# Kernel optimization log

Hardware: AMD Instinct MI355X
Metric: run time of the kernel (lower is better)

Reference implementation:

```python
import jax, jax.numpy as jnp
import numpy as np

N = 65536      # nodes in batched graph
E = 2097152    # edges (avg degree 32)
V = 1000       # chord vocabulary size
F_IN = 128     # chord feature dim
H = 256        # hidden_dim
OUT = 128      # out_dim
G = 256        # number of graphs in batch


def _gcn_layer(x, W, b, row, col, norm, n):
    # x: [n, f_in] -> [n, f_out]; PyG GCNConv: linear then normalized aggregation + bias
    x = x @ W
    msg = x[row] * norm[:, None]            # gather at source, scale by sym-norm
    return jax.ops.segment_sum(msg, col, num_segments=n) + b


def setup_inputs() -> dict:
    key = jax.random.key(0)
    ks = jax.random.split(key, 9)
    chord_feats = jax.random.normal(ks[0], (V, F_IN), jnp.float32)
    W1 = jax.random.normal(ks[1], (F_IN, H), jnp.float32) * 0.05
    b1 = jnp.zeros((H,), jnp.float32)
    W2 = jax.random.normal(ks[2], (H, OUT), jnp.float32) * 0.05
    b2 = jnp.zeros((OUT,), jnp.float32)
    edge_attr = jax.random.uniform(ks[3], (E,), jnp.float32)          # positive edge weights
    node_indices = jax.random.randint(ks[4], (N,), 0, V, jnp.int64)
    edge_index = jax.random.randint(ks[5], (2, E), 0, N, jnp.int64)
    batch_index = jnp.sort(jax.random.randint(ks[6], (N,), 0, G, jnp.int64))
    return {"chord_feats": chord_feats, "W1": W1, "b1": b1, "W2": W2, "b2": b2,
            "edge_attr": edge_attr, "node_indices": node_indices,
            "edge_index": edge_index, "batch_index": batch_index}


def reference(chord_feats, W1, b1, W2, b2, edge_attr, node_indices, edge_index, batch_index):
    loops = jnp.arange(N, dtype=edge_index.dtype)
    row = jnp.concatenate([edge_index[0], loops])   # source
    col = jnp.concatenate([edge_index[1], loops])   # target
    ew = jnp.concatenate([edge_attr, jnp.ones((N,), edge_attr.dtype)])  # self-loop weight 1
    # symmetric GCN normalization: D^-1/2 A D^-1/2
    deg = jax.ops.segment_sum(ew, col, num_segments=N)
    dis = jnp.where(deg > 0, jax.lax.rsqrt(jnp.maximum(deg, 1e-30)), 0.0)
    norm = dis[row] * ew * dis[col]

    x = chord_feats[node_indices]                   # [N, F_IN]
    x = jax.nn.relu(_gcn_layer(x, W1, b1, row, col, norm, N))
    x = jax.nn.relu(_gcn_layer(x, W2, b2, row, col, norm, N))

    # global_mean_pool over batch_index
    sums = jax.ops.segment_sum(x, batch_index, num_segments=G)
    counts = jax.ops.segment_sum(jnp.ones((N,), x.dtype), batch_index, num_segments=G)
    return sums / jnp.maximum(counts, 1.0)[:, None]
```

## Files before the change

### kernel.cpp

```cpp
#include <hip/hip_runtime.h>
#include <hip/hip_fp16.h>
#include <math.h>

constexpr int N_NODES = 65536;
constexpr int N_EDGES = 2097152;
constexpr int F_IN    = 128;
constexpr int H_DIM   = 256;
constexpr int O_DIM   = 128;
constexpr int N_GRAPH = 256;
constexpr int V_SIZE  = 1000;

constexpr int EPB  = 8192;
constexpr int NBLK = N_EDGES / EPB;
constexpr float FXP = 16777216.0f;

typedef _Float16 half8 __attribute__((ext_vector_type(8)));
typedef float floatx4 __attribute__((ext_vector_type(4)));


__global__ void k_init(float* __restrict__ pool, const int* __restrict__ batch,
                       float* __restrict__ cntf, const float* __restrict__ cf,
                       const float* __restrict__ W1, __half* __restrict__ cfW1,
                       const float* __restrict__ W2, _Float16* __restrict__ W2T) {
    __shared__ float xs[8 * F_IN];
    int i = blockIdx.x * blockDim.x + threadIdx.x;
    if (i < N_GRAPH * O_DIM) pool[i] = 0.0f;
    if (blockIdx.x == 0) {
        int g = threadIdx.x;
        int lo = 0, hi = N_NODES;
        while (lo < hi) { int m = (lo + hi) >> 1; if (batch[m] < g) lo = m + 1; else hi = m; }
        int start = lo;
        lo = 0; hi = N_NODES;
        while (lo < hi) { int m = (lo + hi) >> 1; if (batch[m] <= g) lo = m + 1; else hi = m; }
        cntf[g] = (float)(lo - start);
    }
    if (blockIdx.x < V_SIZE / 8) {
        int rb = blockIdx.x * 8;
        int t  = threadIdx.x;
        #pragma unroll
        for (int p = 0; p < 4; ++p) {
            int idx = p * 256 + t;
            int r = idx >> 7, k = idx & 127;
            xs[idx] = cf[(size_t)(rb + r) * F_IN + k];
        }
        __syncthreads();
        float acc[8] = {};
        for (int k = 0; k < F_IN; ++k) {
            float w = W1[k * H_DIM + t];
            #pragma unroll
            for (int j = 0; j < 8; ++j) acc[j] += xs[j * F_IN + k] * w;
        }
        #pragma unroll
        for (int j = 0; j < 8; ++j)
            cfW1[(size_t)(rb + j) * H_DIM + t] = __float2half(acc[j]);
    }
    if (blockIdx.x >= 128) {
        int idx = (blockIdx.x - 128) * 256 + threadIdx.x;
        int nn = idx >> 8, kk = idx & 255;
        W2T[idx] = (_Float16)W2[kk * O_DIM + nn];
    }
}


__global__ void k_hist(const int* __restrict__ col, int* __restrict__ hist) {
    __shared__ int h[256];
    int t = threadIdx.x;
    if (t < 256) h[t] = 0;
    __syncthreads();
    int base = blockIdx.x * EPB;
    #pragma unroll
    for (int i = 0; i < EPB / 1024; ++i)
        atomicAdd(&h[col[base + i * 1024 + t] >> 8], 1);
    __syncthreads();
    if (t < 256) hist[t * NBLK + blockIdx.x] = h[t];
}


__global__ void k_scan1(const int* __restrict__ in, int* __restrict__ out,
                        int* __restrict__ bsum) {
    __shared__ int s[256];
    int tid = threadIdx.x;
    int i = blockIdx.x * 256 + tid;
    int v = in[i];
    s[tid] = v;
    __syncthreads();
    for (int d = 1; d < 256; d <<= 1) {
        int t = (tid >= d) ? s[tid - d] : 0;
        __syncthreads();
        s[tid] += t;
        __syncthreads();
    }
    out[i] = s[tid] - v;
    if (tid == 255) bsum[blockIdx.x] = s[255];
}

__global__ void k_scan2(int* __restrict__ bsum) {
    __shared__ int s[256];
    int tid = threadIdx.x;
    int v = bsum[tid];
    s[tid] = v;
    __syncthreads();
    for (int d = 1; d < 256; d <<= 1) {
        int t = (tid >= d) ? s[tid - d] : 0;
        __syncthreads();
        s[tid] += t;
        __syncthreads();
    }
    bsum[tid] = s[tid] - v;
}


__global__ void k_part(const int* __restrict__ row, const int* __restrict__ col,
                       const float* __restrict__ ew, const int* __restrict__ nidx,
                       const int* __restrict__ hoffs, const int* __restrict__ bsum,
                       int2* __restrict__ part) {
    __shared__ int cur[256];
    int t = threadIdx.x;
    if (t < 256) cur[t] = hoffs[t * NBLK + blockIdx.x] + bsum[t];
    __syncthreads();
    int base = blockIdx.x * EPB;
    #pragma unroll
    for (int i = 0; i < EPB / 1024; ++i) {
        int e = base + i * 1024 + t;
        int r = row[e], c = col[e];
        unsigned hw = (unsigned)__half_as_ushort(__float2half(ew[e]));
        int vb = nidx[r];
        int slot = atomicAdd(&cur[c >> 8], 1);
        int2 rec;
        rec.x = (r << 16) | ((c & 255) << 8) | (vb >> 2);
        rec.y = (int)(((unsigned)(vb & 3) << 16) | hw);
        part[slot] = rec;
    }
}


__global__ void k_build1(const int* __restrict__ hoffs, const int* __restrict__ bsum,
                         const int2* __restrict__ part, float* __restrict__ dis,
                         int* __restrict__ offs) {
    __shared__ unsigned long long dc[256];
    __shared__ int sc[256];
    int t = threadIdx.x;
    int bucket = blockIdx.x;
    if (t < 256) dc[t] = 0ULL;
    __syncthreads();
    int start = hoffs[bucket * NBLK] + bsum[bucket];
    int end   = (bucket == 255) ? N_EDGES : (hoffs[(bucket + 1) * NBLK] + bsum[bucket + 1]);
    for (int j = start + t; j < end; j += 1024) {
        int2 rec = part[j];
        int dst = (rec.x >> 8) & 255;
        float w = __half2float(__ushort_as_half((unsigned short)(rec.y & 0xFFFF)));
        atomicAdd(&dc[dst], (1ULL << 40) |
                  (unsigned long long)(unsigned)(w * FXP + 0.5f));
    }
    __syncthreads();
    unsigned long long v = (t < 256) ? dc[t] : 0ULL;
    if (t < 256) {
        float deg = 1.0f + (float)(v & 0xFFFFFFFFFFULL) * (1.0f / FXP);
        dis[bucket * 256 + t] = 1.0f / sqrtf(deg);
        sc[t] = (int)(v >> 40);
    }
    __syncthreads();
    for (int d = 1; d < 256; d <<= 1) {
        int x = (t >= d && t < 256) ? sc[t - d] : 0;
        __syncthreads();
        if (t < 256) sc[t] += x;
        __syncthreads();
    }
    if (t < 256) {
        int cnt = (int)(v >> 40);
        offs[bucket * 256 + t] = start + sc[t] - cnt;
    }
    if (bucket == 255 && t == 255) offs[N_NODES] = N_EDGES;
}


__global__ void k_build2(const int* __restrict__ hoffs, const int* __restrict__ bsum,
                         const int2* __restrict__ part, const float* __restrict__ dis,
                         const int* __restrict__ offs, int2* __restrict__ csr) {
    __shared__ int cur[256];
    int t = threadIdx.x;
    int bucket = blockIdx.x;
    if (t < 256) cur[t] = offs[bucket * 256 + t];
    __syncthreads();
    int start = hoffs[bucket * NBLK] + bsum[bucket];
    int end   = (bucket == 255) ? N_EDGES : (hoffs[(bucket + 1) * NBLK] + bsum[bucket + 1]);
    for (int j = start + t; j < end; j += 1024) {
        int2 rec = part[j];
        int dst = (rec.x >> 8) & 255;
        unsigned src = ((unsigned)rec.x) >> 16;
        int vb = ((rec.x & 255) << 2) | ((rec.y >> 16) & 3);
        float w = __half2float(__ushort_as_half((unsigned short)(rec.y & 0xFFFF)));
        float nm = dis[src] * w;
        int slot = atomicAdd(&cur[dst], 1);
        int2 e;
        e.x = (int)((src << 10) | (unsigned)vb);
        e.y = __float_as_int(nm);
        csr[slot] = e;
    }
}

__device__ __forceinline__ void acc8(float* e, int4 v, float n) {
    float2 f0 = __half22float2(*(__half2*)&v.x);
    float2 f1 = __half22float2(*(__half2*)&v.y);
    float2 f2 = __half22float2(*(__half2*)&v.z);
    float2 f3 = __half22float2(*(__half2*)&v.w);
    e[0] += f0.x * n; e[1] += f0.y * n;
    e[2] += f1.x * n; e[3] += f1.y * n;
    e[4] += f2.x * n; e[5] += f2.y * n;
    e[6] += f3.x * n; e[7] += f3.y * n;
}


__global__ void k_agg1(const int4* __restrict__ cfW1, const int* __restrict__ nidx,
                       const float* __restrict__ dis, const int* __restrict__ offs,
                       const int2* __restrict__ csr, const float4* __restrict__ b1f4,
                       int4* __restrict__ h1) {
    int wave = threadIdx.x >> 6;
    int lane = threadIdx.x & 63;
    int g    = lane >> 5;
    int sl   = lane & 31;
    int c = blockIdx.x * 4 + wave;
    float d = dis[c];
    int4 sp = cfW1[(size_t)nidx[c] * 32 + sl];
    float esum[8] = {0.f, 0.f, 0.f, 0.f, 0.f, 0.f, 0.f, 0.f};
    int a0 = offs[c], a1 = offs[c + 1];
    int s = a0;
    if (s < a1 && (s & 1)) {
        int sb = __builtin_amdgcn_readfirstlane(s);
        int2 e0 = csr[sb];
        int4 v0 = cfW1[(size_t)(e0.x & 1023) * 32 + sl];
        float n = (g == 0) ? __int_as_float(e0.y) : 0.0f;
        acc8(esum, v0, n);
        ++s;
    }
    for (; s + 8 <= a1; s += 8) {
        int sb = __builtin_amdgcn_readfirstlane(s);
        int4 ee[4];
        #pragma unroll
        for (int u = 0; u < 4; ++u) ee[u] = *(const int4*)(csr + sb + 2 * u);
        int4 v[4]; float n[4];
        #pragma unroll
        for (int u = 0; u < 4; ++u) {
            int ex = g ? ee[u].z : ee[u].x;
            int ey = g ? ee[u].w : ee[u].y;
            n[u] = __int_as_float(ey);
            v[u] = cfW1[(size_t)(ex & 1023) * 32 + sl];
        }
        #pragma unroll
        for (int u = 0; u < 4; ++u) acc8(esum, v[u], n[u]);
    }
    for (; s + 2 <= a1; s += 2) {
        int sb = __builtin_amdgcn_readfirstlane(s);
        int4 ee = *(const int4*)(csr + sb);
        int ex = g ? ee.z : ee.x;
        int ey = g ? ee.w : ee.y;
        int4 v0 = cfW1[(size_t)(ex & 1023) * 32 + sl];
        acc8(esum, v0, __int_as_float(ey));
    }
    if (s < a1) {
        int sb = __builtin_amdgcn_readfirstlane(s);
        int2 e0 = csr[sb];
        int4 v0 = cfW1[(size_t)(e0.x & 1023) * 32 + sl];
        float n = (g == 0) ? __int_as_float(e0.y) : 0.0f;
        acc8(esum, v0, n);
    }
    #pragma unroll
    for (int k = 0; k < 8; ++k) esum[k] += __shfl_xor(esum[k], 32, 64);

    float dd = d * d;
    float2 s0 = __half22float2(*(__half2*)&sp.x);
    float2 s1 = __half22float2(*(__half2*)&sp.y);
    float2 s2 = __half22float2(*(__half2*)&sp.z);
    float2 s3 = __half22float2(*(__half2*)&sp.w);
    float4 bb0 = b1f4[2 * sl];
    float4 bb1 = b1f4[2 * sl + 1];
    float r[8];
    r[0] = bb0.x + s0.x * dd + d * esum[0];
    r[1] = bb0.y + s0.y * dd + d * esum[1];
    r[2] = bb0.z + s1.x * dd + d * esum[2];
    r[3] = bb0.w + s1.y * dd + d * esum[3];
    r[4] = bb1.x + s2.x * dd + d * esum[4];
    r[5] = bb1.y + s2.y * dd + d * esum[5];
    r[6] = bb1.z + s3.x * dd + d * esum[6];
    r[7] = bb1.w + s3.y * dd + d * esum[7];
    #pragma unroll
    for (int k = 0; k < 8; ++k) r[k] = r[k] > 0.f ? r[k] : 0.f;
    float2 p0 = {r[0], r[1]}, p1 = {r[2], r[3]}, p2 = {r[4], r[5]}, p3 = {r[6], r[7]};
    __half2 h0 = __float22half2_rn(p0);
    __half2 h1v = __float22half2_rn(p1);
    __half2 h2 = __float22half2_rn(p2);
    __half2 h3 = __float22half2_rn(p3);
    int4 outv;
    outv.x = *(int*)&h0;
    outv.y = *(int*)&h1v;
    outv.z = *(int*)&h2;
    outv.w = *(int*)&h3;
    if (lane < 32) h1[(size_t)c * 32 + sl] = outv;
}


__global__ void k_gemm2(const _Float16* __restrict__ h1, const _Float16* __restrict__ W2T,
                        __half* __restrict__ xw2h) {
    int wave = threadIdx.x >> 6;
    int lane = threadIdx.x & 63;
    int quad = lane >> 4;
    int n    = lane & 15;
    int tm   = blockIdx.x * 4 + wave;
    const _Float16* arow = h1 + (size_t)(tm * 16 + n) * H_DIM;
    half8 a[8];
    #pragma unroll
    for (int kt = 0; kt < 8; ++kt)
        a[kt] = *(const half8*)(arow + kt * 32 + quad * 8);
    #pragma unroll
    for (int nt = 0; nt < 8; ++nt) {
        floatx4 acc = {0.f, 0.f, 0.f, 0.f};
        const _Float16* brow = W2T + (size_t)(nt * 16 + n) * H_DIM;
        #pragma unroll
        for (int kt = 0; kt < 8; ++kt) {
            half8 b = *(const half8*)(brow + kt * 32 + quad * 8);
            acc = __builtin_amdgcn_mfma_f32_16x16x32_f16(a[kt], b, acc, 0, 0, 0);
        }
        #pragma unroll
        for (int r = 0; r < 4; ++r) {
            int rowi = tm * 16 + quad * 4 + r;
            xw2h[(size_t)rowi * O_DIM + nt * 16 + n] = __float2half(acc[r]);
        }
    }
}


__global__ void k_agg2_pool(const int4* __restrict__ xw2h, const float* __restrict__ b2,
                            const float* __restrict__ dis, const int* __restrict__ offs,
                            const int2* __restrict__ csr, const int* __restrict__ batch,
                            float* __restrict__ pool) {
    __shared__ float red[4][128];
    __shared__ int bgs[4];
    int wave = threadIdx.x >> 6;
    int lane = threadIdx.x & 63;
    int grp  = lane >> 4;
    int sl   = lane & 15;
    int c = blockIdx.x * 4 + wave;
    float d = dis[c];
    int4 sp = xw2h[(size_t)c * 16 + sl];
    float esum[8] = {0.f, 0.f, 0.f, 0.f, 0.f, 0.f, 0.f, 0.f};
    int s0 = offs[c], s1 = offs[c + 1];
    int s = s0;
    for (; s + 16 <= s1; s += 16) {
        int sb = __builtin_amdgcn_readfirstlane(s);
        int2 e[4];
        #pragma unroll
        for (int u = 0; u < 4; ++u) e[u] = csr[sb + 4 * u + grp];
        int4 v[4];
        #pragma unroll
        for (int u = 0; u < 4; ++u)
            v[u] = xw2h[(size_t)(((unsigned)e[u].x) >> 10) * 16 + sl];
        #pragma unroll
        for (int u = 0; u < 4; ++u) acc8(esum, v[u], __int_as_float(e[u].y));
    }
    for (; s + 4 <= s1; s += 4) {
        int sb = __builtin_amdgcn_readfirstlane(s);
        int2 e0 = csr[sb + grp];
        int4 v0 = xw2h[(size_t)(((unsigned)e0.x) >> 10) * 16 + sl];
        acc8(esum, v0, __int_as_float(e0.y));
    }
    if (s < s1) {
        int sb = __builtin_amdgcn_readfirstlane(s);
        int idx = sb + grp;
        int idc = idx < s1 ? idx : s1 - 1;
        int2 e0 = csr[idc];
        int4 v0 = xw2h[(size_t)(((unsigned)e0.x) >> 10) * 16 + sl];
        float n = (idx < s1) ? __int_as_float(e0.y) : 0.0f;
        acc8(esum, v0, n);
    }
    #pragma unroll
    for (int k = 0; k < 8; ++k) {
        esum[k] += __shfl_xor(esum[k], 16, 64);
        esum[k] += __shfl_xor(esum[k], 32, 64);
    }
    float dd = d * d;
    float2 f0 = __half22float2(*(__half2*)&sp.x);
    float2 f1 = __half22float2(*(__half2*)&sp.y);
    float2 f2 = __half22float2(*(__half2*)&sp.z);
    float2 f3 = __half22float2(*(__half2*)&sp.w);
    float4 bb0 = ((const float4*)b2)[2 * sl];
    float4 bb1 = ((const float4*)b2)[2 * sl + 1];
    float acc[8];
    acc[0] = bb0.x + f0.x * dd + d * esum[0];
    acc[1] = bb0.y + f0.y * dd + d * esum[1];
    acc[2] = bb0.z + f1.x * dd + d * esum[2];
    acc[3] = bb0.w + f1.y * dd + d * esum[3];
    acc[4] = bb1.x + f2.x * dd + d * esum[4];
    acc[5] = bb1.y + f2.y * dd + d * esum[5];
    acc[6] = bb1.z + f3.x * dd + d * esum[6];
    acc[7] = bb1.w + f3.y * dd + d * esum[7];
    #pragma unroll
    for (int k = 0; k < 8; ++k) acc[k] = acc[k] > 0.f ? acc[k] : 0.f;
    if (grp == 0) {
        #pragma unroll
        for (int k = 0; k < 8; ++k) red[wave][8 * sl + k] = acc[k];
    }
    if (lane == 0) bgs[wave] = batch[c];
    __syncthreads();
    if (wave == 0) {
        float2 a;
        a.x = red[0][2 * lane];
        a.y = red[0][2 * lane + 1];
        int cg = bgs[0];
        #pragma unroll
        for (int w = 1; w < 4; ++w) {
            int g = bgs[w];
            float2 r;
            r.x = red[w][2 * lane];
            r.y = red[w][2 * lane + 1];
            if (g == cg) { a.x += r.x; a.y += r.y; }
            else {
                atomicAdd(&pool[cg * O_DIM + 2 * lane], a.x);
                atomicAdd(&pool[cg * O_DIM + 2 * lane + 1], a.y);
                a = r; cg = g;
            }
        }
        atomicAdd(&pool[cg * O_DIM + 2 * lane], a.x);
        atomicAdd(&pool[cg * O_DIM + 2 * lane + 1], a.y);
    }
}

__global__ void k_final(const float* __restrict__ pool, const float* __restrict__ cnt,
                        float* __restrict__ out) {
    int t = blockIdx.x * blockDim.x + threadIdx.x;
    if (t < N_GRAPH * O_DIM) {
        int g = t / O_DIM;
        out[t] = pool[t] / fmaxf(cnt[g], 1.0f);
    }
}


extern "C" void kernel_launch(void* const* d_in, const int* in_sizes, int n_in,
                              void* d_out, int out_size, void* d_ws, size_t ws_size,
                              hipStream_t stream) {
    const float* cf   = (const float*)d_in[0];
    const float* W1   = (const float*)d_in[1];
    const float* b1   = (const float*)d_in[2];
    const float* W2   = (const float*)d_in[3];
    const float* b2   = (const float*)d_in[4];
    const float* ew   = (const float*)d_in[5];
    const int*   nidx = (const int*)d_in[6];
    const int*   eidx = (const int*)d_in[7];
    const int*   bidx = (const int*)d_in[8];
    float* out = (float*)d_out;

    const int* row = eidx;
    const int* col = eidx + N_EDGES;

    char* ws = (char*)d_ws;
    size_t off = 0;
    int*   hist  = (int*)  (ws + off); off += (size_t)N_NODES * 4;
    int*   hoffs = (int*)  (ws + off); off += (size_t)N_NODES * 4;
    int*   bsum  = (int*)  (ws + off); off += 4096;
    float* dis   = (float*)(ws + off); off += (size_t)N_NODES * 4;
    int*   offs  = (int*)  (ws + off); off += (size_t)(N_NODES + 16) * 4;
    int2*  csr   = (int2*) (ws + off); off += (size_t)N_EDGES * 8;
    float* pool  = (float*)(ws + off); off += (size_t)(N_GRAPH * O_DIM + N_GRAPH) * 4;
    __half* cfW1 = (__half*)(ws + off); off += (size_t)V_SIZE * H_DIM * 2;
    _Float16* W2T = (_Float16*)(ws + off); off += (size_t)O_DIM * H_DIM * 2;
    off = (off + 255) & ~(size_t)255;
    int2*  part  = (int2*) (ws + off); off += (size_t)N_EDGES * 8;
    __half* h1   = (__half*)(ws + off);
    __half* xw2h = (__half*)part;
    float* cntf  = pool + N_GRAPH * O_DIM;

    k_init<<<256, 256, 0, stream>>>(pool, bidx, cntf, cf, W1, cfW1, W2, W2T);
    k_hist<<<NBLK, 1024, 0, stream>>>(col, hist);
    k_scan1<<<256, 256, 0, stream>>>(hist, hoffs, bsum);
    k_scan2<<<1, 256, 0, stream>>>(bsum);

    k_part<<<NBLK, 1024, 0, stream>>>(row, col, ew, nidx, hoffs, bsum, part);
    k_build1<<<256, 1024, 0, stream>>>(hoffs, bsum, part, dis, offs);
    k_build2<<<256, 1024, 0, stream>>>(hoffs, bsum, part, dis, offs, csr);

    k_agg1<<<N_NODES / 4, 256, 0, stream>>>((const int4*)cfW1, nidx, dis, offs, csr,
                                            (const float4*)b1, (int4*)h1);

    k_gemm2<<<N_NODES / 64, 256, 0, stream>>>((const _Float16*)h1, W2T, xw2h);
    k_agg2_pool<<<N_NODES / 4, 256, 0, stream>>>((const int4*)xw2h, b2, dis, offs, csr,
                                                 bidx, pool);

    k_final<<<(N_GRAPH * O_DIM + 255) / 256, 256, 0, stream>>>(pool, cntf, out);
}
```

Measured before the change: 321.3 us.

## Split CSR build into quarter-bucket blocks and halve edges per partition block

Halves edges per partition block so twice as many blocks run the histogram and partition passes. The scan is widened to match, with the second scan handling two sums per thread. The degree/offset build kernel is split into three: a degree counter where each bucket is handled by four blocks that each own a quarter of the destinations, a separate per-bucket prefix-scan kernel, and a quarter-bucket CSR scatter. This raises parallelism from 256 to 1024 blocks, but each block now reads the whole bucket's partition and discards three quarters of it. Degree accumulation moves to a 32-bit fixed point with 16 fractional bits, which loses precision and risks overflow if a node's weight sum exceeds 256.

```diff
diff --git a/kernel.cpp b/kernel.cpp
--- a/kernel.cpp
+++ b/kernel.cpp
@@ -10,9 +10,8 @@
 constexpr int N_GRAPH = 256;
 constexpr int V_SIZE  = 1000;
 
-constexpr int EPB  = 8192;
+constexpr int EPB  = 4096;
 constexpr int NBLK = N_EDGES / EPB;
-constexpr float FXP = 16777216.0f;
 
 typedef _Float16 half8 __attribute__((ext_vector_type(8)));
 typedef float floatx4 __attribute__((ext_vector_type(4)));
@@ -96,17 +95,20 @@
 
 __global__ void k_scan2(int* __restrict__ bsum) {
     __shared__ int s[256];
-    int tid = threadIdx.x;
-    int v = bsum[tid];
-    s[tid] = v;
+    int t = threadIdx.x;
+    int2 v = *(int2*)&bsum[2 * t];
+    int tsum = v.x + v.y;
+    s[t] = tsum;
     __syncthreads();
     for (int d = 1; d < 256; d <<= 1) {
-        int t = (tid >= d) ? s[tid - d] : 0;
-        __syncthreads();
-        s[tid] += t;
-        __syncthreads();
-    }
-    bsum[tid] = s[tid] - v;
+        int x = (t >= d) ? s[t - d] : 0;
+        __syncthreads();
+        s[t] += x;
+        __syncthreads();
+    }
+    int ex = s[t] - tsum;
+    bsum[2 * t]     = ex;
+    bsum[2 * t + 1] = ex + v.x;
 }
 
 
@@ -116,7 +118,10 @@
                        int2* __restrict__ part) {
     __shared__ int cur[256];
     int t = threadIdx.x;
-    if (t < 256) cur[t] = hoffs[t * NBLK + blockIdx.x] + bsum[t];
+    if (t < 256) {
+        int idx = t * NBLK + blockIdx.x;
+        cur[t] = hoffs[idx] + bsum[idx >> 8];
+    }
     __syncthreads();
     int base = blockIdx.x * EPB;
     #pragma unroll
@@ -134,68 +139,79 @@
 }
 
 
-__global__ void k_build1(const int* __restrict__ hoffs, const int* __restrict__ bsum,
-                         const int2* __restrict__ part, float* __restrict__ dis,
-                         int* __restrict__ offs) {
-    __shared__ unsigned long long dc[256];
+__global__ void k_degq(const int* __restrict__ hoffs, const int* __restrict__ bsum,
+                       const int2* __restrict__ part, unsigned* __restrict__ dcq) {
+    __shared__ unsigned dc[64];
+    int t = threadIdx.x;
+    int bucket = blockIdx.x & 255, q = blockIdx.x >> 8;
+    if (t < 64) dc[t] = 0u;
+    __syncthreads();
+    int start = hoffs[bucket * NBLK] + bsum[bucket * 2];
+    int end   = (bucket == 255) ? N_EDGES
+                                : (hoffs[(bucket + 1) * NBLK] + bsum[(bucket + 1) * 2]);
+    for (int j = start + t; j < end; j += 1024) {
+        int2 rec = part[j];
+        int dst = (rec.x >> 8) & 255;
+        if ((dst >> 6) == q) {
+            float w = __half2float(__ushort_as_half((unsigned short)(rec.y & 0xFFFF)));
+            atomicAdd(&dc[dst & 63], (1u << 24) | (unsigned)(w * 65536.0f + 0.5f));
+        }
+    }
+    __syncthreads();
+    if (t < 64) dcq[bucket * 256 + q * 64 + t] = dc[t];
+}
+
+
+__global__ void k_disoffs(const unsigned* __restrict__ dcq,
+                          const int* __restrict__ hoffs, const int* __restrict__ bsum,
+                          float* __restrict__ dis, int* __restrict__ offs) {
     __shared__ int sc[256];
     int t = threadIdx.x;
     int bucket = blockIdx.x;
-    if (t < 256) dc[t] = 0ULL;
-    __syncthreads();
-    int start = hoffs[bucket * NBLK] + bsum[bucket];
-    int end   = (bucket == 255) ? N_EDGES : (hoffs[(bucket + 1) * NBLK] + bsum[bucket + 1]);
+    unsigned v = dcq[bucket * 256 + t];
+    float wsum = (float)(v & 0xFFFFFFu) * (1.0f / 65536.0f);
+    float deg = 1.0f + wsum;
+    dis[bucket * 256 + t] = 1.0f / sqrtf(deg);
+    int cnt = (int)(v >> 24);
+    int bstart = hoffs[bucket * NBLK] + bsum[bucket * 2];
+    sc[t] = cnt;
+    __syncthreads();
+    for (int d = 1; d < 256; d <<= 1) {
+        int x = (t >= d) ? sc[t - d] : 0;
+        __syncthreads();
+        sc[t] += x;
+        __syncthreads();
+    }
+    offs[bucket * 256 + t] = bstart + sc[t] - cnt;
+    if (bucket == 255 && t == 255) offs[N_NODES] = N_EDGES;
+}
+
+
+__global__ void k_build2q(const int* __restrict__ hoffs, const int* __restrict__ bsum,
+                          const int2* __restrict__ part, const float* __restrict__ dis,
+                          const int* __restrict__ offs, int2* __restrict__ csr) {
+    __shared__ int cur[64];
+    int t = threadIdx.x;
+    int bucket = blockIdx.x & 255, q = blockIdx.x >> 8;
+    if (t < 64) cur[t] = offs[bucket * 256 + q * 64 + t];
+    __syncthreads();
+    int start = hoffs[bucket * NBLK] + bsum[bucket * 2];
+    int end   = (bucket == 255) ? N_EDGES
+                                : (hoffs[(bucket + 1) * NBLK] + bsum[(bucket + 1) * 2]);
     for (int j = start + t; j < end; j += 1024) {
         int2 rec = part[j];
         int dst = (rec.x >> 8) & 255;
-        float w = __half2float(__ushort_as_half((unsigned short)(rec.y & 0xFFFF)));
-        atomicAdd(&dc[dst], (1ULL << 40) |
-                  (unsigned long long)(unsigned)(w * FXP + 0.5f));
-    }
-    __syncthreads();
-    unsigned long long v = (t < 256) ? dc[t] : 0ULL;
-    if (t < 256) {
-        float deg = 1.0f + (float)(v & 0xFFFFFFFFFFULL) * (1.0f / FXP);
-        dis[bucket * 256 + t] = 1.0f / sqrtf(deg);
-        sc[t] = (int)(v >> 40);
-    }
-    __syncthreads();
-    for (int d = 1; d < 256; d <<= 1) {
-        int x = (t >= d && t < 256) ? sc[t - d] : 0;
-        __syncthreads();
-        if (t < 256) sc[t] += x;
-        __syncthreads();
-    }
-    if (t < 256) {
-        int cnt = (int)(v >> 40);
-        offs[bucket * 256 + t] = start + sc[t] - cnt;
-    }
-    if (bucket == 255 && t == 255) offs[N_NODES] = N_EDGES;
-}
-
-
-__global__ void k_build2(const int* __restrict__ hoffs, const int* __restrict__ bsum,
-                         const int2* __restrict__ part, const float* __restrict__ dis,
-                         const int* __restrict__ offs, int2* __restrict__ csr) {
-    __shared__ int cur[256];
-    int t = threadIdx.x;
-    int bucket = blockIdx.x;
-    if (t < 256) cur[t] = offs[bucket * 256 + t];
-    __syncthreads();
-    int start = hoffs[bucket * NBLK] + bsum[bucket];
-    int end   = (bucket == 255) ? N_EDGES : (hoffs[(bucket + 1) * NBLK] + bsum[bucket + 1]);
-    for (int j = start + t; j < end; j += 1024) {
-        int2 rec = part[j];
-        int dst = (rec.x >> 8) & 255;
-        unsigned src = ((unsigned)rec.x) >> 16;
-        int vb = ((rec.x & 255) << 2) | ((rec.y >> 16) & 3);
-        float w = __half2float(__ushort_as_half((unsigned short)(rec.y & 0xFFFF)));
-        float nm = dis[src] * w;
-        int slot = atomicAdd(&cur[dst], 1);
-        int2 e;
-        e.x = (int)((src << 10) | (unsigned)vb);
-        e.y = __float_as_int(nm);
-        csr[slot] = e;
+        if ((dst >> 6) == q) {
+            unsigned src = ((unsigned)rec.x) >> 16;
+            int vb = ((rec.x & 255) << 2) | ((rec.y >> 16) & 3);
+            float w = __half2float(__ushort_as_half((unsigned short)(rec.y & 0xFFFF)));
+            float nm = dis[src] * w;
+            int slot = atomicAdd(&cur[dst & 63], 1);
+            int2 e;
+            e.x = (int)((src << 10) | (unsigned)vb);
+            e.y = __float_as_int(nm);
+            csr[slot] = e;
+        }
     }
 }
 
@@ -453,9 +469,10 @@
 
     char* ws = (char*)d_ws;
     size_t off = 0;
-    int*   hist  = (int*)  (ws + off); off += (size_t)N_NODES * 4;
-    int*   hoffs = (int*)  (ws + off); off += (size_t)N_NODES * 4;
-    int*   bsum  = (int*)  (ws + off); off += 4096;
+    int*   hist  = (int*)  (ws + off); off += (size_t)256 * NBLK * 4;
+    int*   hoffs = (int*)  (ws + off); off += (size_t)256 * NBLK * 4;
+    int*   bsum  = (int*)  (ws + off); off += (size_t)NBLK * 4;
+    unsigned* dcq = (unsigned*)(ws + off); off += (size_t)N_NODES * 4;
     float* dis   = (float*)(ws + off); off += (size_t)N_NODES * 4;
     int*   offs  = (int*)  (ws + off); off += (size_t)(N_NODES + 16) * 4;
     int2*  csr   = (int2*) (ws + off); off += (size_t)N_EDGES * 8;
@@ -470,12 +487,13 @@
 
     k_init<<<256, 256, 0, stream>>>(pool, bidx, cntf, cf, W1, cfW1, W2, W2T);
     k_hist<<<NBLK, 1024, 0, stream>>>(col, hist);
-    k_scan1<<<256, 256, 0, stream>>>(hist, hoffs, bsum);
+    k_scan1<<<256 * NBLK / 256, 256, 0, stream>>>(hist, hoffs, bsum);
     k_scan2<<<1, 256, 0, stream>>>(bsum);
 
     k_part<<<NBLK, 1024, 0, stream>>>(row, col, ew, nidx, hoffs, bsum, part);
-    k_build1<<<256, 1024, 0, stream>>>(hoffs, bsum, part, dis, offs);
-    k_build2<<<256, 1024, 0, stream>>>(hoffs, bsum, part, dis, offs, csr);
+    k_degq<<<1024, 1024, 0, stream>>>(hoffs, bsum, part, dcq);
+    k_disoffs<<<256, 256, 0, stream>>>(dcq, hoffs, bsum, dis, offs);
+    k_build2q<<<1024, 1024, 0, stream>>>(hoffs, bsum, part, dis, offs, csr);
 
     k_agg1<<<N_NODES / 4, 256, 0, stream>>>((const int4*)cfW1, nidx, dis, offs, csr,
                                             (const float4*)b1, (int4*)h1);
```

Result: slower. 333.1 us (+3.7%).

## Merge init with histogram, fold bsum scan into consumers, unroll agg1 deeper

Applied to the files above, without the earlier changes.

Fuses the init kernel and the edge histogram into one 1024-thread launch, and removes the separate single-block scan2 launch by having each of k_part, k_build1 and k_build2 redundantly scan the 256 block sums in shared memory. This cuts two kernel launches and their serialization gaps. It also doubles the edge unroll in k_agg1 to 16 edges per iteration with launch bounds for more loads in flight, at the cost of extra register pressure and redundant scan work per block.

```diff
diff --git a/kernel.cpp b/kernel.cpp
--- a/kernel.cpp
+++ b/kernel.cpp
@@ -18,15 +18,31 @@
 typedef float floatx4 __attribute__((ext_vector_type(4)));
 
 
-__global__ void k_init(float* __restrict__ pool, const int* __restrict__ batch,
-                       float* __restrict__ cntf, const float* __restrict__ cf,
-                       const float* __restrict__ W1, __half* __restrict__ cfW1,
-                       const float* __restrict__ W2, _Float16* __restrict__ W2T) {
+__global__ void k_init_hist(float* __restrict__ pool, const int* __restrict__ batch,
+                            float* __restrict__ cntf, const float* __restrict__ cf,
+                            const float* __restrict__ W1, __half* __restrict__ cfW1,
+                            const float* __restrict__ W2, _Float16* __restrict__ W2T,
+                            const int* __restrict__ col, int* __restrict__ hist) {
     __shared__ float xs[8 * F_IN];
-    int i = blockIdx.x * blockDim.x + threadIdx.x;
+    __shared__ int h[256];
+    int b = blockIdx.x;
+    int t = threadIdx.x;
+    if (b >= 256) {
+        int eb = b - 256;
+        if (t < 256) h[t] = 0;
+        __syncthreads();
+        int base = eb * EPB;
+        #pragma unroll
+        for (int i = 0; i < EPB / 1024; ++i)
+            atomicAdd(&h[col[base + i * 1024 + t] >> 8], 1);
+        __syncthreads();
+        if (t < 256) hist[t * NBLK + eb] = h[t];
+        return;
+    }
+    int i = b * 1024 + t;
     if (i < N_GRAPH * O_DIM) pool[i] = 0.0f;
-    if (blockIdx.x == 0) {
-        int g = threadIdx.x;
+    if (b == 0 && t < 256) {
+        int g = t;
         int lo = 0, hi = N_NODES;
         while (lo < hi) { int m = (lo + hi) >> 1; if (batch[m] < g) lo = m + 1; else hi = m; }
         int start = lo;
@@ -34,45 +50,27 @@
         while (lo < hi) { int m = (lo + hi) >> 1; if (batch[m] <= g) lo = m + 1; else hi = m; }
         cntf[g] = (float)(lo - start);
     }
-    if (blockIdx.x < V_SIZE / 8) {
-        int rb = blockIdx.x * 8;
-        int t  = threadIdx.x;
-        #pragma unroll
-        for (int p = 0; p < 4; ++p) {
-            int idx = p * 256 + t;
-            int r = idx >> 7, k = idx & 127;
-            xs[idx] = cf[(size_t)(rb + r) * F_IN + k];
+    if (b < V_SIZE / 8) {
+        int rb = b * 8;
+        xs[t] = cf[(size_t)(rb + (t >> 7)) * F_IN + (t & 127)];
+        __syncthreads();
+        int ct = t & 255, g2 = t >> 8;
+        float a0 = 0.f, a1 = 0.f;
+        const float* x0 = &xs[(g2 * 2) * F_IN];
+        const float* x1 = &xs[(g2 * 2 + 1) * F_IN];
+        for (int k = 0; k < F_IN; ++k) {
+            float w = W1[k * H_DIM + ct];
+            a0 += x0[k] * w;
+            a1 += x1[k] * w;
         }
-        __syncthreads();
-        float acc[8] = {};
-        for (int k = 0; k < F_IN; ++k) {
-            float w = W1[k * H_DIM + t];
-            #pragma unroll
-            for (int j = 0; j < 8; ++j) acc[j] += xs[j * F_IN + k] * w;
-        }
-        #pragma unroll
-        for (int j = 0; j < 8; ++j)
-            cfW1[(size_t)(rb + j) * H_DIM + t] = __float2half(acc[j]);
-    }
-    if (blockIdx.x >= 128) {
-        int idx = (blockIdx.x - 128) * 256 + threadIdx.x;
+        cfW1[(size_t)(rb + g2 * 2) * H_DIM + ct]     = __float2half(a0);
+        cfW1[(size_t)(rb + g2 * 2 + 1) * H_DIM + ct] = __float2half(a1);
+    }
+    if (b >= 128 && b < 160) {
+        int idx = (b - 128) * 1024 + t;
         int nn = idx >> 8, kk = idx & 255;
         W2T[idx] = (_Float16)W2[kk * O_DIM + nn];
     }
-}
-
-
-__global__ void k_hist(const int* __restrict__ col, int* __restrict__ hist) {
-    __shared__ int h[256];
-    int t = threadIdx.x;
-    if (t < 256) h[t] = 0;
-    __syncthreads();
-    int base = blockIdx.x * EPB;
-    #pragma unroll
-    for (int i = 0; i < EPB / 1024; ++i)
-        atomicAdd(&h[col[base + i * 1024 + t] >> 8], 1);
-    __syncthreads();
-    if (t < 256) hist[t * NBLK + blockIdx.x] = h[t];
 }
 
 
@@ -94,19 +92,20 @@
     if (tid == 255) bsum[blockIdx.x] = s[255];
 }
 
-__global__ void k_scan2(int* __restrict__ bsum) {
-    __shared__ int s[256];
-    int tid = threadIdx.x;
-    int v = bsum[tid];
-    s[tid] = v;
+__device__ __forceinline__ void scan_bsum(const int* __restrict__ bsum,
+                                          int* __restrict__ sbuf,
+                                          int* __restrict__ exc, int t) {
+    if (t < 256) sbuf[t] = bsum[t];
     __syncthreads();
     for (int d = 1; d < 256; d <<= 1) {
-        int t = (tid >= d) ? s[tid - d] : 0;
-        __syncthreads();
-        s[tid] += t;
-        __syncthreads();
-    }
-    bsum[tid] = s[tid] - v;
+        int x = (t < 256 && t >= d) ? sbuf[t - d] : 0;
+        __syncthreads();
+        if (t < 256) sbuf[t] += x;
+        __syncthreads();
+    }
+    if (t < 256) exc[t + 1] = sbuf[t];
+    if (t == 0) exc[0] = 0;
+    __syncthreads();
 }
 
 
@@ -115,8 +114,11 @@
                        const int* __restrict__ hoffs, const int* __restrict__ bsum,
                        int2* __restrict__ part) {
     __shared__ int cur[256];
+    __shared__ int sbuf[256];
+    __shared__ int exc[257];
     int t = threadIdx.x;
-    if (t < 256) cur[t] = hoffs[t * NBLK + blockIdx.x] + bsum[t];
+    scan_bsum(bsum, sbuf, exc, t);
+    if (t < 256) cur[t] = hoffs[t * NBLK + blockIdx.x] + exc[t];
     __syncthreads();
     int base = blockIdx.x * EPB;
     #pragma unroll
@@ -139,12 +141,15 @@
                          int* __restrict__ offs) {
     __shared__ unsigned long long dc[256];
     __shared__ int sc[256];
+    __shared__ int sbuf[256];
+    __shared__ int exc[257];
     int t = threadIdx.x;
     int bucket = blockIdx.x;
+    scan_bsum(bsum, sbuf, exc, t);
     if (t < 256) dc[t] = 0ULL;
     __syncthreads();
-    int start = hoffs[bucket * NBLK] + bsum[bucket];
-    int end   = (bucket == 255) ? N_EDGES : (hoffs[(bucket + 1) * NBLK] + bsum[bucket + 1]);
+    int start = hoffs[bucket * NBLK] + exc[bucket];
+    int end   = (bucket == 255) ? N_EDGES : (hoffs[(bucket + 1) * NBLK] + exc[bucket + 1]);
     for (int j = start + t; j < end; j += 1024) {
         int2 rec = part[j];
         int dst = (rec.x >> 8) & 255;
@@ -178,12 +183,15 @@
                          const int2* __restrict__ part, const float* __restrict__ dis,
                          const int* __restrict__ offs, int2* __restrict__ csr) {
     __shared__ int cur[256];
+    __shared__ int sbuf[256];
+    __shared__ int exc[257];
     int t = threadIdx.x;
     int bucket = blockIdx.x;
+    scan_bsum(bsum, sbuf, exc, t);
     if (t < 256) cur[t] = offs[bucket * 256 + t];
     __syncthreads();
-    int start = hoffs[bucket * NBLK] + bsum[bucket];
-    int end   = (bucket == 255) ? N_EDGES : (hoffs[(bucket + 1) * NBLK] + bsum[bucket + 1]);
+    int start = hoffs[bucket * NBLK] + exc[bucket];
+    int end   = (bucket == 255) ? N_EDGES : (hoffs[(bucket + 1) * NBLK] + exc[bucket + 1]);
     for (int j = start + t; j < end; j += 1024) {
         int2 rec = part[j];
         int dst = (rec.x >> 8) & 255;
@@ -211,10 +219,11 @@
 }
 
 
-__global__ void k_agg1(const int4* __restrict__ cfW1, const int* __restrict__ nidx,
-                       const float* __restrict__ dis, const int* __restrict__ offs,
-                       const int2* __restrict__ csr, const float4* __restrict__ b1f4,
-                       int4* __restrict__ h1) {
+__global__ void __launch_bounds__(256, 4) k_agg1(
+        const int4* __restrict__ cfW1, const int* __restrict__ nidx,
+        const float* __restrict__ dis, const int* __restrict__ offs,
+        const int2* __restrict__ csr, const float4* __restrict__ b1f4,
+        int4* __restrict__ h1) {
     int wave = threadIdx.x >> 6;
     int lane = threadIdx.x & 63;
     int g    = lane >> 5;
@@ -233,7 +242,23 @@
         acc8(esum, v0, n);
         ++s;
     }
-    for (; s + 8 <= a1; s += 8) {
+    for (; s + 16 <= a1; s += 16) {
+        int sb = __builtin_amdgcn_readfirstlane(s);
+        int4 ee[8];
+        #pragma unroll
+        for (int u = 0; u < 8; ++u) ee[u] = *(const int4*)(csr + sb + 2 * u);
+        int4 v[8]; float n[8];
+        #pragma unroll
+        for (int u = 0; u < 8; ++u) {
+            int ex = g ? ee[u].z : ee[u].x;
+            int ey = g ? ee[u].w : ee[u].y;
+            n[u] = __int_as_float(ey);
+            v[u] = cfW1[(size_t)(ex & 1023) * 32 + sl];
+        }
+        #pragma unroll
+        for (int u = 0; u < 8; ++u) acc8(esum, v[u], n[u]);
+    }
+    if (s + 8 <= a1) {
         int sb = __builtin_amdgcn_readfirstlane(s);
         int4 ee[4];
         #pragma unroll
@@ -248,6 +273,7 @@
         }
         #pragma unroll
         for (int u = 0; u < 4; ++u) acc8(esum, v[u], n[u]);
+        s += 8;
     }
     for (; s + 2 <= a1; s += 2) {
         int sb = __builtin_amdgcn_readfirstlane(s);
@@ -468,10 +494,9 @@
     __half* xw2h = (__half*)part;
     float* cntf  = pool + N_GRAPH * O_DIM;
 
-    k_init<<<256, 256, 0, stream>>>(pool, bidx, cntf, cf, W1, cfW1, W2, W2T);
-    k_hist<<<NBLK, 1024, 0, stream>>>(col, hist);
+    k_init_hist<<<512, 1024, 0, stream>>>(pool, bidx, cntf, cf, W1, cfW1, W2, W2T,
+                                          col, hist);
     k_scan1<<<256, 256, 0, stream>>>(hist, hoffs, bsum);
-    k_scan2<<<1, 256, 0, stream>>>(bsum);
 
     k_part<<<NBLK, 1024, 0, stream>>>(row, col, ew, nidx, hoffs, bsum, part);
     k_build1<<<256, 1024, 0, stream>>>(hoffs, bsum, part, dis, offs);
```

Result: slower. 332.6 us (+3.5%).

## Fuse scan, partition and CSR build into one cooperative kernel

Applied to the files above, without the earlier changes.

Merges the two scan kernels, the partition pass and both CSR build passes into a single cooperative kernel that uses grid-wide syncs instead of separate launches. NBLK is 256, so one block of 1024 threads covers each histogram row and each bucket. If the cooperative launch fails, the old kernels run instead, each now scanning the block sums itself in shared memory. The aim is to cut launch gaps and tail idling between the small stages. The cost is grid-sync overhead and a requirement that all 256 blocks of 1024 threads be resident at once.

```diff
diff --git a/kernel.cpp b/kernel.cpp
--- a/kernel.cpp
+++ b/kernel.cpp
@@ -1,6 +1,9 @@
 #include <hip/hip_runtime.h>
 #include <hip/hip_fp16.h>
+#include <hip/hip_cooperative_groups.h>
 #include <math.h>
+
+namespace cg = cooperative_groups;
 
 constexpr int N_NODES = 65536;
 constexpr int N_EDGES = 2097152;
@@ -76,6 +79,115 @@
 }
 
 
+__global__ void __launch_bounds__(1024) k_prep(
+        const int* __restrict__ hist, int* __restrict__ hoffs, int* __restrict__ bsum,
+        const int* __restrict__ row, const int* __restrict__ col,
+        const float* __restrict__ ew, const int* __restrict__ nidx,
+        int2* __restrict__ part, float* __restrict__ dis,
+        int* __restrict__ offs, int2* __restrict__ csr) {
+    __shared__ int sbuf[256];
+    __shared__ int exc[257];
+    __shared__ int cur[256];
+    __shared__ unsigned long long dc[256];
+    __shared__ int sc[256];
+    cg::grid_group grid = cg::this_grid();
+    int t = threadIdx.x;
+    int b = blockIdx.x;
+
+    int v0 = 0;
+    if (t < 256) { v0 = hist[b * 256 + t]; sbuf[t] = v0; }
+    __syncthreads();
+    for (int d = 1; d < 256; d <<= 1) {
+        int x = (t < 256 && t >= d) ? sbuf[t - d] : 0;
+        __syncthreads();
+        if (t < 256) sbuf[t] += x;
+        __syncthreads();
+    }
+    if (t < 256) hoffs[b * 256 + t] = sbuf[t] - v0;
+    if (t == 255) bsum[b] = sbuf[255];
+    grid.sync();
+
+    if (t < 256) sbuf[t] = bsum[t];
+    __syncthreads();
+    for (int d = 1; d < 256; d <<= 1) {
+        int x = (t < 256 && t >= d) ? sbuf[t - d] : 0;
+        __syncthreads();
+        if (t < 256) sbuf[t] += x;
+        __syncthreads();
+    }
+    if (t < 256) exc[t + 1] = sbuf[t];
+    if (t == 0) exc[0] = 0;
+    __syncthreads();
+
+    if (t < 256) cur[t] = hoffs[t * NBLK + b] + exc[t];
+    __syncthreads();
+    {
+        int base = b * EPB;
+        #pragma unroll
+        for (int i = 0; i < EPB / 1024; ++i) {
+            int e = base + i * 1024 + t;
+            int r = row[e], c = col[e];
+            unsigned hw = (unsigned)__half_as_ushort(__float2half(ew[e]));
+            int vb = nidx[r];
+            int slot = atomicAdd(&cur[c >> 8], 1);
+            int2 rec;
+            rec.x = (r << 16) | ((c & 255) << 8) | (vb >> 2);
+            rec.y = (int)(((unsigned)(vb & 3) << 16) | hw);
+            part[slot] = rec;
+        }
+    }
+    grid.sync();
+
+    int start = exc[b];
+    int end   = exc[b + 1];
+    if (t < 256) dc[t] = 0ULL;
+    __syncthreads();
+    for (int j = start + t; j < end; j += 1024) {
+        int2 rec = part[j];
+        int dst = (rec.x >> 8) & 255;
+        float w = __half2float(__ushort_as_half((unsigned short)(rec.y & 0xFFFF)));
+        atomicAdd(&dc[dst], (1ULL << 40) |
+                  (unsigned long long)(unsigned)(w * FXP + 0.5f));
+    }
+    __syncthreads();
+    unsigned long long v = (t < 256) ? dc[t] : 0ULL;
+    if (t < 256) {
+        float deg = 1.0f + (float)(v & 0xFFFFFFFFFFULL) * (1.0f / FXP);
+        dis[b * 256 + t] = 1.0f / sqrtf(deg);
+        sc[t] = (int)(v >> 40);
+    }
+    __syncthreads();
+    for (int d = 1; d < 256; d <<= 1) {
+        int x = (t >= d && t < 256) ? sc[t - d] : 0;
+        __syncthreads();
+        if (t < 256) sc[t] += x;
+        __syncthreads();
+    }
+    if (t < 256) {
+        int cnt = (int)(v >> 40);
+        offs[b * 256 + t] = start + sc[t] - cnt;
+    }
+    if (b == 255 && t == 255) offs[N_NODES] = N_EDGES;
+    grid.sync();
+
+    if (t < 256) cur[t] = offs[b * 256 + t];
+    __syncthreads();
+    for (int j = start + t; j < end; j += 1024) {
+        int2 rec = part[j];
+        int dst = (rec.x >> 8) & 255;
+        unsigned src = ((unsigned)rec.x) >> 16;
+        int vb = ((rec.x & 255) << 2) | ((rec.y >> 16) & 3);
+        float w = __half2float(__ushort_as_half((unsigned short)(rec.y & 0xFFFF)));
+        float nm = dis[src] * w;
+        int slot = atomicAdd(&cur[dst], 1);
+        int2 e;
+        e.x = (int)((src << 10) | (unsigned)vb);
+        e.y = __float_as_int(nm);
+        csr[slot] = e;
+    }
+}
+
+
 __global__ void k_scan1(const int* __restrict__ in, int* __restrict__ out,
                         int* __restrict__ bsum) {
     __shared__ int s[256];
@@ -94,29 +206,32 @@
     if (tid == 255) bsum[blockIdx.x] = s[255];
 }
 
-__global__ void k_scan2(int* __restrict__ bsum) {
-    __shared__ int s[256];
-    int tid = threadIdx.x;
-    int v = bsum[tid];
-    s[tid] = v;
+__device__ __forceinline__ void scan_bsum(const int* __restrict__ bsum,
+                                          int* __restrict__ sbuf,
+                                          int* __restrict__ exc, int t) {
+    if (t < 256) sbuf[t] = bsum[t];
     __syncthreads();
     for (int d = 1; d < 256; d <<= 1) {
-        int t = (tid >= d) ? s[tid - d] : 0;
-        __syncthreads();
-        s[tid] += t;
-        __syncthreads();
-    }
-    bsum[tid] = s[tid] - v;
-}
-
+        int x = (t < 256 && t >= d) ? sbuf[t - d] : 0;
+        __syncthreads();
+        if (t < 256) sbuf[t] += x;
+        __syncthreads();
+    }
+    if (t < 256) exc[t + 1] = sbuf[t];
+    if (t == 0) exc[0] = 0;
+    __syncthreads();
+}
 
 __global__ void k_part(const int* __restrict__ row, const int* __restrict__ col,
                        const float* __restrict__ ew, const int* __restrict__ nidx,
                        const int* __restrict__ hoffs, const int* __restrict__ bsum,
                        int2* __restrict__ part) {
     __shared__ int cur[256];
+    __shared__ int sbuf[256];
+    __shared__ int exc[257];
     int t = threadIdx.x;
-    if (t < 256) cur[t] = hoffs[t * NBLK + blockIdx.x] + bsum[t];
+    scan_bsum(bsum, sbuf, exc, t);
+    if (t < 256) cur[t] = hoffs[t * NBLK + blockIdx.x] + exc[t];
     __syncthreads();
     int base = blockIdx.x * EPB;
     #pragma unroll
@@ -133,18 +248,20 @@
     }
 }
 
-
 __global__ void k_build1(const int* __restrict__ hoffs, const int* __restrict__ bsum,
                          const int2* __restrict__ part, float* __restrict__ dis,
                          int* __restrict__ offs) {
     __shared__ unsigned long long dc[256];
     __shared__ int sc[256];
+    __shared__ int sbuf[256];
+    __shared__ int exc[257];
     int t = threadIdx.x;
     int bucket = blockIdx.x;
+    scan_bsum(bsum, sbuf, exc, t);
     if (t < 256) dc[t] = 0ULL;
     __syncthreads();
-    int start = hoffs[bucket * NBLK] + bsum[bucket];
-    int end   = (bucket == 255) ? N_EDGES : (hoffs[(bucket + 1) * NBLK] + bsum[bucket + 1]);
+    int start = exc[bucket];
+    int end   = exc[bucket + 1];
     for (int j = start + t; j < end; j += 1024) {
         int2 rec = part[j];
         int dst = (rec.x >> 8) & 255;
@@ -173,17 +290,19 @@
     if (bucket == 255 && t == 255) offs[N_NODES] = N_EDGES;
 }
 
-
 __global__ void k_build2(const int* __restrict__ hoffs, const int* __restrict__ bsum,
                          const int2* __restrict__ part, const float* __restrict__ dis,
                          const int* __restrict__ offs, int2* __restrict__ csr) {
     __shared__ int cur[256];
+    __shared__ int sbuf[256];
+    __shared__ int exc[257];
     int t = threadIdx.x;
     int bucket = blockIdx.x;
+    scan_bsum(bsum, sbuf, exc, t);
     if (t < 256) cur[t] = offs[bucket * 256 + t];
     __syncthreads();
-    int start = hoffs[bucket * NBLK] + bsum[bucket];
-    int end   = (bucket == 255) ? N_EDGES : (hoffs[(bucket + 1) * NBLK] + bsum[bucket + 1]);
+    int start = exc[bucket];
+    int end   = exc[bucket + 1];
     for (int j = start + t; j < end; j += 1024) {
         int2 rec = part[j];
         int dst = (rec.x >> 8) & 255;
@@ -470,12 +589,21 @@
 
     k_init<<<256, 256, 0, stream>>>(pool, bidx, cntf, cf, W1, cfW1, W2, W2T);
     k_hist<<<NBLK, 1024, 0, stream>>>(col, hist);
-    k_scan1<<<256, 256, 0, stream>>>(hist, hoffs, bsum);
-    k_scan2<<<1, 256, 0, stream>>>(bsum);
-
-    k_part<<<NBLK, 1024, 0, stream>>>(row, col, ew, nidx, hoffs, bsum, part);
-    k_build1<<<256, 1024, 0, stream>>>(hoffs, bsum, part, dis, offs);
-    k_build2<<<256, 1024, 0, stream>>>(hoffs, bsum, part, dis, offs, csr);
+
+    {
+        const int* hist_c = hist;
+        void* args[] = {(void*)&hist_c, (void*)&hoffs, (void*)&bsum,
+                        (void*)&row, (void*)&col, (void*)&ew, (void*)&nidx,
+                        (void*)&part, (void*)&dis, (void*)&offs, (void*)&csr};
+        hipError_t err = hipLaunchCooperativeKernel((const void*)k_prep, dim3(256),
+                                                    dim3(1024), args, 0, stream);
+        if (err != hipSuccess) {
+            k_scan1<<<256, 256, 0, stream>>>(hist, hoffs, bsum);
+            k_part<<<NBLK, 1024, 0, stream>>>(row, col, ew, nidx, hoffs, bsum, part);
+            k_build1<<<256, 1024, 0, stream>>>(hoffs, bsum, part, dis, offs);
+            k_build2<<<256, 1024, 0, stream>>>(hoffs, bsum, part, dis, offs, csr);
+        }
+    }
 
     k_agg1<<<N_NODES / 4, 256, 0, stream>>>((const int4*)cfW1, nidx, dis, offs, csr,
                                             (const float4*)b1, (int4*)h1);
```

New measurement: 427.3 us. 33.0% more time.
